# Optimization experiments

Measured on AMD Instinct MI355X. Metric: run time of the kernel, lower is better.

## Reference

```python
import jax, jax.numpy as jnp
import numpy as np

CUTOFF = 8.0
NUM_RBF = 16
N = 2048
NUM_GRAPHS = 16


def setup_inputs() -> dict:
    key = jax.random.key(0)
    k1, k2 = jax.random.split(key)
    pos = jax.random.normal(k1, (N, 3), dtype=jnp.float32)
    batch = jnp.sort(jax.random.randint(k2, (N,), 0, NUM_GRAPHS)).astype(jnp.int64)
    # buffers from __init__
    centers = jnp.linspace(0.0, CUTOFF, NUM_RBF).astype(jnp.float32)
    width = jnp.asarray(CUTOFF / NUM_RBF * 0.5, dtype=jnp.float32)
    return {"pos": pos, "batch": batch, "centers": centers, "width": width}


def reference(pos, batch, centers, width):
    # Dense jit-friendly equivalent of the torch module: instead of filtering
    # pairs to a data-dependent edge list, we keep the full [N, N] pair grid
    # and return a boolean validity mask plus RBF features zeroed where invalid.
    n = pos.shape[0]
    idx = jnp.arange(n)
    diff = pos[:, None, :] - pos[None, :, :] + 1e-10  # [N, N, 3] (torch adds 1e-10 to diff)
    dist = jnp.sqrt(jnp.sum(diff * diff, axis=-1))     # [N, N]
    mask = (idx[:, None] != idx[None, :]) \
        & (batch[:, None] == batch[None, :]) \
        & (dist < CUTOFF)                               # [N, N] valid-edge mask
    # RBF encoding: exp(-(d - c)^2 / (2 w^2)), zeroed for invalid pairs
    rbf = jnp.exp(-((dist[..., None] - centers) ** 2) / (2.0 * width ** 2))  # [N, N, R]
    rbf = rbf * mask[..., None].astype(rbf.dtype)
    return mask, rbf
```

## Files before the change

### kernel.cpp

```cpp
#include <hip/hip_runtime.h>
#include <hip/hip_bf16.h>


constexpr int N    = 2048;
constexpr int NRBF = 16;

typedef float  f32x4  __attribute__((ext_vector_type(4)));
typedef short  s16x8  __attribute__((ext_vector_type(8)));

__device__ inline float bf16_bits_to_f32(unsigned short h) {
    union { unsigned int u; float f; } c;
    c.u = ((unsigned int)h) << 16;
    return c.f;
}

__device__ inline short f32_to_bf16_bits(float f) {
    __hip_bfloat16 b = __float2bfloat16(f);
    union { __hip_bfloat16 b; short s; } c; c.b = b;
    return c.s;
}

__device__ inline float pair_dist(float xi, float yi, float zi,
                                  float xj, float yj, float zj) {
    const float dx = __fadd_rn(__fsub_rn(xi, xj), 1e-10f);
    const float dy = __fadd_rn(__fsub_rn(yi, yj), 1e-10f);
    const float dz = __fadd_rn(__fsub_rn(zi, zj), 1e-10f);
    const float d2 = __fadd_rn(__fadd_rn(__fmul_rn(dx, dx), __fmul_rn(dy, dy)),
                               __fmul_rn(dz, dz));
    return __fsqrt_rn(d2);
}

__global__ __launch_bounds__(256) void edge_rbf_kernel(
    const void* __restrict__ pos_raw,
    const int*  __restrict__ batch32,
    const void* __restrict__ centers_raw,
    const void* __restrict__ width_raw,
    void*       __restrict__ out_raw)
{
    const int lane = threadIdx.x & 63;
    const int wv   = threadIdx.x >> 6;
    const int i    = blockIdx.y;
    const int j0   = blockIdx.x * 256 + wv * 64;
    const int jL   = j0 + lane;

    const unsigned int* posw = (const unsigned int*)pos_raw;
    int cnt = 0;
#pragma unroll
    for (int k = 0; k < 16; ++k) {
        float v = bf16_bits_to_f32((unsigned short)(posw[k] & 0xFFFFu));
        float a = fabsf(v);
        if (a > 1e-6f && a < 100.0f) ++cnt;
    }
    const bool is_bf16 = (cnt >= 12);
    const bool b64 = (batch32[N - 1] == 0);

    const int bi  = b64 ? batch32[2 * i]  : batch32[i];
    const int bjL = b64 ? batch32[2 * jL] : batch32[jL];
    const bool beqL = (bi == bjL) && (i != jL);

    const unsigned long long eligible = __ballot(beqL);

    const size_t row = (size_t)i * N;

    if (eligible == 0ull) {
        if (is_bf16) {
            short* mask_out = (short*)out_raw;
            short* rbf_out  = mask_out + (size_t)N * N;
            __builtin_nontemporal_store((short)0, mask_out + row + jL);
            s16x8 z = (s16x8)0;
            short* base = rbf_out + (row + j0) * NRBF;
#pragma unroll
            for (int q = 0; q < 2; ++q)
                __builtin_nontemporal_store(
                    z, (s16x8*)(base + q * 512 + lane * 8));
        } else {
            float* mask_out = (float*)out_raw;
            float* rbf_out  = mask_out + (size_t)N * N;
            __builtin_nontemporal_store(0.0f, mask_out + row + jL);
            f32x4 z = (f32x4)0.0f;
            float* base = rbf_out + (row + j0) * NRBF;
#pragma unroll
            for (int q = 0; q < 4; ++q)
                __builtin_nontemporal_store(
                    z, (f32x4*)(base + q * 256 + lane * 4));
        }
        return;
    }

    float xi, yi, zi, w;
    float cen[NRBF];
    if (is_bf16) {
        const __hip_bfloat16* pos     = (const __hip_bfloat16*)pos_raw;
        const __hip_bfloat16* centers = (const __hip_bfloat16*)centers_raw;
        const __hip_bfloat16* width   = (const __hip_bfloat16*)width_raw;
        xi = __bfloat162float(pos[3 * i + 0]);
        yi = __bfloat162float(pos[3 * i + 1]);
        zi = __bfloat162float(pos[3 * i + 2]);
        w  = __bfloat162float(width[0]);
#pragma unroll
        for (int r = 0; r < NRBF; ++r) cen[r] = __bfloat162float(centers[r]);
    } else {
        const float* pos     = (const float*)pos_raw;
        const float* centers = (const float*)centers_raw;
        const float* width   = (const float*)width_raw;
        xi = pos[3 * i + 0];  yi = pos[3 * i + 1];  zi = pos[3 * i + 2];
        w  = width[0];
#pragma unroll
        for (int r = 0; r < NRBF; ++r) cen[r] = centers[r];
    }
    const float ninv = -1.0f / (2.0f * w * w);

    float xjL, yjL, zjL;
    if (is_bf16) {
        const __hip_bfloat16* pos = (const __hip_bfloat16*)pos_raw;
        xjL = __bfloat162float(pos[3 * jL + 0]);
        yjL = __bfloat162float(pos[3 * jL + 1]);
        zjL = __bfloat162float(pos[3 * jL + 2]);
    } else {
        const float* pos = (const float*)pos_raw;
        xjL = pos[3 * jL + 0];  yjL = pos[3 * jL + 1];  zjL = pos[3 * jL + 2];
    }
    const float dL     = pair_dist(xi, yi, zi, xjL, yjL, zjL);
    const bool  validL = beqL && (dL < 8.0f);

    if (is_bf16) {
        short* mask_out = (short*)out_raw;
        short* rbf_out  = mask_out + (size_t)N * N;
        __builtin_nontemporal_store(f32_to_bf16_bits(validL ? 1.0f : 0.0f),
                                    mask_out + row + jL);

        const __hip_bfloat16* pos = (const __hip_bfloat16*)pos_raw;
        short* base = rbf_out + (row + j0) * NRBF;
#pragma unroll
        for (int q = 0; q < 2; ++q) {
            const int p  = q * 32 + (lane >> 1);
            const int c0 = (lane & 1) * 8;
            const int jp = j0 + p;
            const float xj = __bfloat162float(pos[3 * jp + 0]);
            const float yj = __bfloat162float(pos[3 * jp + 1]);
            const float zj = __bfloat162float(pos[3 * jp + 2]);
            const float d  = pair_dist(xi, yi, zi, xj, yj, zj);
            const bool  ok = ((eligible >> p) & 1ull) && (d < 8.0f);
            s16x8 o;
#pragma unroll
            for (int t = 0; t < 8; ++t) {
                const float tt = d - cen[c0 + t];
                o[t] = f32_to_bf16_bits(ok ? __expf(tt * tt * ninv) : 0.0f);
            }
            __builtin_nontemporal_store(o, (s16x8*)(base + q * 512 + lane * 8));
        }
    } else {
        float* mask_out = (float*)out_raw;
        float* rbf_out  = mask_out + (size_t)N * N;
        __builtin_nontemporal_store(validL ? 1.0f : 0.0f, mask_out + row + jL);

        const float* pos = (const float*)pos_raw;
        float* base = rbf_out + (row + j0) * NRBF;
#pragma unroll
        for (int q = 0; q < 4; ++q) {
            const int p  = q * 16 + (lane >> 2);
            const int c0 = (lane & 3) * 4;
            const int jp = j0 + p;
            const float xj = pos[3 * jp + 0];
            const float yj = pos[3 * jp + 1];
            const float zj = pos[3 * jp + 2];
            const float d  = pair_dist(xi, yi, zi, xj, yj, zj);
            const bool  ok = ((eligible >> p) & 1ull) && (d < 8.0f);
            f32x4 o;
#pragma unroll
            for (int t = 0; t < 4; ++t) {
                const float tt = d - cen[c0 + t];
                o[t] = ok ? __expf(tt * tt * ninv) : 0.0f;
            }
            __builtin_nontemporal_store(o, (f32x4*)(base + q * 256 + lane * 4));
        }
    }
}

extern "C" void kernel_launch(void* const* d_in, const int* in_sizes, int n_in,
                              void* d_out, int out_size, void* d_ws, size_t ws_size,
                              hipStream_t stream) {
    const void* pos     = d_in[0];
    const int*  batch   = (const int*)d_in[1];
    const void* centers = d_in[2];
    const void* width   = d_in[3];

    dim3 grid(N / 256, N);
    dim3 block(256);
    edge_rbf_kernel<<<grid, block, 0, stream>>>(pos, batch, centers, width,
                                                d_out);
}
```

Measured before the change: 287.1 us.

## Process whole row per block using binary-searched graph range to skip zero tiles

Each block now handles one full output row i and loops over all column tiles. A binary search over the sorted batch array gives the graph's [lo,hi) range, so tiles entirely outside it take a zero-store fast path without loading batch or positions. The grid shrinks from 8×2048 to 2048 blocks, which cuts per-block setup (dtype probe, batch-width check) and relies on the batch array being sorted. The trade-off is a serial loop per block and a small binary-search cost, which may reduce memory-level parallelism for a kernel that is mostly bound by store bandwidth.

```diff
diff --git a/kernel.cpp b/kernel.cpp
--- a/kernel.cpp
+++ b/kernel.cpp
@@ -2,8 +2,9 @@
 #include <hip/hip_bf16.h>
 
 
-constexpr int N    = 2048;
-constexpr int NRBF = 16;
+constexpr int N     = 2048;
+constexpr int NRBF  = 16;
+constexpr int NTILE = N / 256;
 
 typedef float  f32x4  __attribute__((ext_vector_type(4)));
 typedef short  s16x8  __attribute__((ext_vector_type(8)));
@@ -39,9 +40,7 @@
 {
     const int lane = threadIdx.x & 63;
     const int wv   = threadIdx.x >> 6;
-    const int i    = blockIdx.y;
-    const int j0   = blockIdx.x * 256 + wv * 64;
-    const int jL   = j0 + lane;
+    const int i    = blockIdx.x;
 
     const unsigned int* posw = (const unsigned int*)pos_raw;
     int cnt = 0;
@@ -54,125 +53,146 @@
     const bool is_bf16 = (cnt >= 12);
     const bool b64 = (batch32[N - 1] == 0);
 
-    const int bi  = b64 ? batch32[2 * i]  : batch32[i];
-    const int bjL = b64 ? batch32[2 * jL] : batch32[jL];
-    const bool beqL = (bi == bjL) && (i != jL);
-
-    const unsigned long long eligible = __ballot(beqL);
+    const int g = b64 ? batch32[2 * i] : batch32[i];
+    int lo, hi;
+    {
+        int l = 0, h = N;
+        while (l < h) {
+            int m  = (l + h) >> 1;
+            int bm = b64 ? batch32[2 * m] : batch32[m];
+            if (bm < g) l = m + 1; else h = m;
+        }
+        lo = l;
+        h = N;
+        while (l < h) {
+            int m  = (l + h) >> 1;
+            int bm = b64 ? batch32[2 * m] : batch32[m];
+            if (bm <= g) l = m + 1; else h = m;
+        }
+        hi = l;
+    }
 
     const size_t row = (size_t)i * N;
 
-    if (eligible == 0ull) {
-        if (is_bf16) {
-            short* mask_out = (short*)out_raw;
-            short* rbf_out  = mask_out + (size_t)N * N;
-            __builtin_nontemporal_store((short)0, mask_out + row + jL);
-            s16x8 z = (s16x8)0;
-            short* base = rbf_out + (row + j0) * NRBF;
-#pragma unroll
-            for (int q = 0; q < 2; ++q)
-                __builtin_nontemporal_store(
-                    z, (s16x8*)(base + q * 512 + lane * 8));
-        } else {
-            float* mask_out = (float*)out_raw;
-            float* rbf_out  = mask_out + (size_t)N * N;
-            __builtin_nontemporal_store(0.0f, mask_out + row + jL);
-            f32x4 z = (f32x4)0.0f;
-            float* base = rbf_out + (row + j0) * NRBF;
-#pragma unroll
-            for (int q = 0; q < 4; ++q)
-                __builtin_nontemporal_store(
-                    z, (f32x4*)(base + q * 256 + lane * 4));
-        }
-        return;
-    }
-
-    float xi, yi, zi, w;
-    float cen[NRBF];
     if (is_bf16) {
         const __hip_bfloat16* pos     = (const __hip_bfloat16*)pos_raw;
         const __hip_bfloat16* centers = (const __hip_bfloat16*)centers_raw;
         const __hip_bfloat16* width   = (const __hip_bfloat16*)width_raw;
-        xi = __bfloat162float(pos[3 * i + 0]);
-        yi = __bfloat162float(pos[3 * i + 1]);
-        zi = __bfloat162float(pos[3 * i + 2]);
-        w  = __bfloat162float(width[0]);
+        short* mask_out = (short*)out_raw;
+        short* rbf_out  = mask_out + (size_t)N * N;
+
+        const float xi = __bfloat162float(pos[3 * i + 0]);
+        const float yi = __bfloat162float(pos[3 * i + 1]);
+        const float zi = __bfloat162float(pos[3 * i + 2]);
+        const float w  = __bfloat162float(width[0]);
+        float cen[NRBF];
 #pragma unroll
         for (int r = 0; r < NRBF; ++r) cen[r] = __bfloat162float(centers[r]);
+        const float ninv = -1.0f / (2.0f * w * w);
+
+        for (int t = 0; t < NTILE; ++t) {
+            const int jt = t * 256 + wv * 64;
+            const int jL = jt + lane;
+            short* base = rbf_out + (row + jt) * NRBF;
+
+            if (jt + 64 <= lo || jt >= hi) {
+                __builtin_nontemporal_store((short)0, mask_out + row + jL);
+                s16x8 z = (s16x8)0;
+#pragma unroll
+                for (int q = 0; q < 2; ++q)
+                    __builtin_nontemporal_store(
+                        z, (s16x8*)(base + q * 512 + lane * 8));
+                continue;
+            }
+
+            const bool eligL = (jL >= lo) && (jL < hi) && (jL != i);
+            const float xjL = __bfloat162float(pos[3 * jL + 0]);
+            const float yjL = __bfloat162float(pos[3 * jL + 1]);
+            const float zjL = __bfloat162float(pos[3 * jL + 2]);
+            const float dL  = pair_dist(xi, yi, zi, xjL, yjL, zjL);
+            const bool validL = eligL && (dL < 8.0f);
+            __builtin_nontemporal_store(f32_to_bf16_bits(validL ? 1.0f : 0.0f),
+                                        mask_out + row + jL);
+
+#pragma unroll
+            for (int q = 0; q < 2; ++q) {
+                const int p  = q * 32 + (lane >> 1);
+                const int c0 = (lane & 1) * 8;
+                const int jp = jt + p;
+                const float xj = __bfloat162float(pos[3 * jp + 0]);
+                const float yj = __bfloat162float(pos[3 * jp + 1]);
+                const float zj = __bfloat162float(pos[3 * jp + 2]);
+                const float d  = pair_dist(xi, yi, zi, xj, yj, zj);
+                const bool  ok = (jp >= lo) && (jp < hi) && (jp != i)
+                                 && (d < 8.0f);
+                s16x8 o;
+#pragma unroll
+                for (int u = 0; u < 8; ++u) {
+                    const float tt = d - cen[c0 + u];
+                    o[u] = f32_to_bf16_bits(ok ? __expf(tt * tt * ninv) : 0.0f);
+                }
+                __builtin_nontemporal_store(o, (s16x8*)(base + q * 512 + lane * 8));
+            }
+        }
     } else {
         const float* pos     = (const float*)pos_raw;
         const float* centers = (const float*)centers_raw;
         const float* width   = (const float*)width_raw;
-        xi = pos[3 * i + 0];  yi = pos[3 * i + 1];  zi = pos[3 * i + 2];
-        w  = width[0];
-#pragma unroll
-        for (int r = 0; r < NRBF; ++r) cen[r] = centers[r];
-    }
-    const float ninv = -1.0f / (2.0f * w * w);
-
-    float xjL, yjL, zjL;
-    if (is_bf16) {
-        const __hip_bfloat16* pos = (const __hip_bfloat16*)pos_raw;
-        xjL = __bfloat162float(pos[3 * jL + 0]);
-        yjL = __bfloat162float(pos[3 * jL + 1]);
-        zjL = __bfloat162float(pos[3 * jL + 2]);
-    } else {
-        const float* pos = (const float*)pos_raw;
-        xjL = pos[3 * jL + 0];  yjL = pos[3 * jL + 1];  zjL = pos[3 * jL + 2];
-    }
-    const float dL     = pair_dist(xi, yi, zi, xjL, yjL, zjL);
-    const bool  validL = beqL && (dL < 8.0f);
-
-    if (is_bf16) {
-        short* mask_out = (short*)out_raw;
-        short* rbf_out  = mask_out + (size_t)N * N;
-        __builtin_nontemporal_store(f32_to_bf16_bits(validL ? 1.0f : 0.0f),
-                                    mask_out + row + jL);
-
-        const __hip_bfloat16* pos = (const __hip_bfloat16*)pos_raw;
-        short* base = rbf_out + (row + j0) * NRBF;
-#pragma unroll
-        for (int q = 0; q < 2; ++q) {
-            const int p  = q * 32 + (lane >> 1);
-            const int c0 = (lane & 1) * 8;
-            const int jp = j0 + p;
-            const float xj = __bfloat162float(pos[3 * jp + 0]);
-            const float yj = __bfloat162float(pos[3 * jp + 1]);
-            const float zj = __bfloat162float(pos[3 * jp + 2]);
-            const float d  = pair_dist(xi, yi, zi, xj, yj, zj);
-            const bool  ok = ((eligible >> p) & 1ull) && (d < 8.0f);
-            s16x8 o;
-#pragma unroll
-            for (int t = 0; t < 8; ++t) {
-                const float tt = d - cen[c0 + t];
-                o[t] = f32_to_bf16_bits(ok ? __expf(tt * tt * ninv) : 0.0f);
-            }
-            __builtin_nontemporal_store(o, (s16x8*)(base + q * 512 + lane * 8));
-        }
-    } else {
         float* mask_out = (float*)out_raw;
         float* rbf_out  = mask_out + (size_t)N * N;
-        __builtin_nontemporal_store(validL ? 1.0f : 0.0f, mask_out + row + jL);
-
-        const float* pos = (const float*)pos_raw;
-        float* base = rbf_out + (row + j0) * NRBF;
-#pragma unroll
-        for (int q = 0; q < 4; ++q) {
-            const int p  = q * 16 + (lane >> 2);
-            const int c0 = (lane & 3) * 4;
-            const int jp = j0 + p;
-            const float xj = pos[3 * jp + 0];
-            const float yj = pos[3 * jp + 1];
-            const float zj = pos[3 * jp + 2];
-            const float d  = pair_dist(xi, yi, zi, xj, yj, zj);
-            const bool  ok = ((eligible >> p) & 1ull) && (d < 8.0f);
-            f32x4 o;
-#pragma unroll
-            for (int t = 0; t < 4; ++t) {
-                const float tt = d - cen[c0 + t];
-                o[t] = ok ? __expf(tt * tt * ninv) : 0.0f;
-            }
-            __builtin_nontemporal_store(o, (f32x4*)(base + q * 256 + lane * 4));
+
+        const float xi = pos[3 * i + 0];
+        const float yi = pos[3 * i + 1];
+        const float zi = pos[3 * i + 2];
+        const float w  = width[0];
+        float cen[NRBF];
+#pragma unroll
+        for (int r = 0; r < NRBF; ++r) cen[r] = centers[r];
+        const float ninv = -1.0f / (2.0f * w * w);
+
+        for (int t = 0; t < NTILE; ++t) {
+            const int jt = t * 256 + wv * 64;
+            const int jL = jt + lane;
+            float* base = rbf_out + (row + jt) * NRBF;
+
+            if (jt + 64 <= lo || jt >= hi) {
+                __builtin_nontemporal_store(0.0f, mask_out + row + jL);
+                f32x4 z = (f32x4)0.0f;
+#pragma unroll
+                for (int q = 0; q < 4; ++q)
+                    __builtin_nontemporal_store(
+                        z, (f32x4*)(base + q * 256 + lane * 4));
+                continue;
+            }
+
+            const bool eligL = (jL >= lo) && (jL < hi) && (jL != i);
+            const float xjL = pos[3 * jL + 0];
+            const float yjL = pos[3 * jL + 1];
+            const float zjL = pos[3 * jL + 2];
+            const float dL  = pair_dist(xi, yi, zi, xjL, yjL, zjL);
+            const bool validL = eligL && (dL < 8.0f);
+            __builtin_nontemporal_store(validL ? 1.0f : 0.0f,
+                                        mask_out + row + jL);
+
+#pragma unroll
+            for (int q = 0; q < 4; ++q) {
+                const int p  = q * 16 + (lane >> 2);
+                const int c0 = (lane & 3) * 4;
+                const int jp = jt + p;
+                const float xj = pos[3 * jp + 0];
+                const float yj = pos[3 * jp + 1];
+                const float zj = pos[3 * jp + 2];
+                const float d  = pair_dist(xi, yi, zi, xj, yj, zj);
+                const bool  ok = (jp >= lo) && (jp < hi) && (jp != i)
+                                 && (d < 8.0f);
+                f32x4 o;
+#pragma unroll
+                for (int u = 0; u < 4; ++u) {
+                    const float tt = d - cen[c0 + u];
+                    o[u] = ok ? __expf(tt * tt * ninv) : 0.0f;
+                }
+                __builtin_nontemporal_store(o, (f32x4*)(base + q * 256 + lane * 4));
+            }
         }
     }
 }
@@ -185,7 +205,7 @@
     const void* centers = d_in[2];
     const void* width   = d_in[3];
 
-    dim3 grid(N / 256, N);
+    dim3 grid(N);
     dim3 block(256);
     edge_rbf_kernel<<<grid, block, 0, stream>>>(pos, batch, centers, width,
                                                 d_out);
```

After: 289.6 us. No clear change (+0.9%).
